# Kernel tuning notes

Measured on AMD Instinct MI355X. Metric: run time of the kernel, lower is better.

The kernel has to match this reference:

```python
import jax, jax.numpy as jnp
import numpy as np

D_MODEL = 1024
NUM_HEADS = 16
BATCH = 2
SEQ = 2048


def setup_inputs() -> dict:
    key = jax.random.key(0)
    ks = jax.random.split(key, 5)
    scale = 1.0 / np.sqrt(D_MODEL)
    x = jax.random.normal(ks[0], (BATCH, SEQ, D_MODEL), dtype=jnp.float32)
    Wq = jax.random.normal(ks[1], (D_MODEL, D_MODEL), dtype=jnp.float32) * scale
    Wk = jax.random.normal(ks[2], (D_MODEL, D_MODEL), dtype=jnp.float32) * scale
    Wv = jax.random.normal(ks[3], (D_MODEL, D_MODEL), dtype=jnp.float32) * scale
    Wo = jax.random.normal(ks[4], (D_MODEL, D_MODEL), dtype=jnp.float32) * scale
    return {"x": x, "Wq": Wq, "Wk": Wk, "Wv": Wv, "Wo": Wo}


def reference(x, Wq, Wk, Wv, Wo):
    b, s, d_model = x.shape
    h = NUM_HEADS
    d_head = d_model // h
    # projections (Linear with weight [out,in]: y = x @ W^T)
    def split_heads(y):
        return y.reshape(b, s, h, d_head).transpose(0, 2, 1, 3)  # b h s d
    q = split_heads(x @ Wq.T)
    k = split_heads(x @ Wk.T)
    v = split_heads(x @ Wv.T)
    # full (non-flash) attention, as in the original
    att = jnp.einsum('bhsd,bhtd->bhst', q, k) / jnp.sqrt(jnp.float32(d_head)).astype(x.dtype)
    att = jax.nn.softmax(att, axis=-1)
    out = jnp.einsum('bhst,bhtd->bhsd', att, v)
    out = out.transpose(0, 2, 1, 3).reshape(b, s, d_model)
    return out @ Wo.T
```

## Files before the change

kernel.cpp:

```cpp
#include <hip/hip_runtime.h>
#include <stdint.h>

typedef __bf16 bf16_t;
typedef __bf16 bf16x4 __attribute__((ext_vector_type(4)));
typedef __bf16 bf16x8 __attribute__((ext_vector_type(8)));
typedef float  f32x4  __attribute__((ext_vector_type(4)));
typedef float  f32x16 __attribute__((ext_vector_type(16)));

#define D_MODEL 1024
#define SEQ     2048
#define BATCH   2
#define NHEAD   16
#define DHEAD   64
#define NROWS   (BATCH*SEQ)
#define LDT     72

#define QSCALE  (0.125f * 1.4426950408889634f)

__device__ __forceinline__ void async_ld16(const bf16_t* g, bf16_t* l) {
    __builtin_amdgcn_global_load_lds(
        (const __attribute__((address_space(1))) uint32_t*)(uintptr_t)g,
        (__attribute__((address_space(3))) uint32_t*)(uintptr_t)l,
        16, 0, 0);
}

__device__ __forceinline__ bf16x8 cvt8(f32x4 lo, f32x4 hi) {
    bf16x8 o;
#pragma unroll
    for (int i = 0; i < 4; ++i) { o[i] = (bf16_t)lo[i]; o[4 + i] = (bf16_t)hi[i]; }
    return o;
}

__device__ __forceinline__ bf16x4 shflx32(bf16x4 v) {
    union { bf16x4 b; long long u; } x;
    x.b = v;
    x.u = __shfl_xor(x.u, 32);
    return x.b;
}

__global__ void __launch_bounds__(256)
k_cvt(const float* __restrict__ w0, const float* __restrict__ w1,
      const float* __restrict__ w2, const float* __restrict__ w3,
      const float* __restrict__ x,
      bf16_t* __restrict__ o0, bf16_t* __restrict__ o1,
      bf16_t* __restrict__ o2, bf16_t* __restrict__ o3,
      bf16_t* __restrict__ ox)
{
    const int blk = blockIdx.x;
    const float* s; bf16_t* d; int bi;
    if (blk < 2048) { s = x; d = ox; bi = blk; }
    else {
        const int t = blk - 2048, sel = t >> 9; bi = t & 511;
        s = (sel == 0) ? w0 : (sel == 1) ? w1 : (sel == 2) ? w2 : w3;
        d = (sel == 0) ? o0 : (sel == 1) ? o1 : (sel == 2) ? o2 : o3;
    }
    const size_t i = ((size_t)bi * 256 + threadIdx.x) * 8;
    *(bf16x8*)(d + i) = cvt8(*(const f32x4*)(s + i), *(const f32x4*)(s + i + 4));
}

template <int OUT_MODE>
__device__ __forceinline__ void gemm128(bf16_t* __restrict__ smem,
                                        const bf16_t* __restrict__ X,
                                        const bf16_t* __restrict__ W,
                                        void* __restrict__ Yv,
                                        int m0, int n0, float oscale)
{
    bf16_t* lA = smem;
    bf16_t* lB = smem + 128 * 32;

    const int tid  = threadIdx.x;
    const int lane = tid & 63;
    const int w    = tid >> 6;
    const int l15  = lane & 15;
    const int quad = lane >> 4;

    const int c0 = tid, c1 = tid + 256;
    const int r0 = c0 >> 2, r1 = c1 >> 2;
    const int kc0 = (c0 & 3) ^ ((r0 >> 1) & 3);
    const int kc1 = (c1 & 3) ^ ((r1 >> 1) & 3);
    const bf16_t* gA0 = X + (size_t)(m0 + r0) * D_MODEL + kc0 * 8;
    const bf16_t* gA1 = X + (size_t)(m0 + r1) * D_MODEL + kc1 * 8;
    const bf16_t* gB0 = W + (size_t)(n0 + r0) * D_MODEL + kc0 * 8;
    const bf16_t* gB1 = W + (size_t)(n0 + r1) * D_MODEL + kc1 * 8;

    int am[4], bn[4];
    const int mw = (w >> 1) * 64, nw = (w & 1) * 64;
#pragma unroll
    for (int i = 0; i < 4; ++i) {
        const int ra = mw + i * 16 + l15;
        am[i] = ra * 32 + (quad ^ ((ra >> 1) & 3)) * 8;
        const int rb = nw + i * 16 + l15;
        bn[i] = rb * 32 + (quad ^ ((rb >> 1) & 3)) * 8;
    }

    f32x4 acc[4][4];
#pragma unroll
    for (int i = 0; i < 4; ++i)
#pragma unroll
        for (int j = 0; j < 4; ++j) acc[i][j] = f32x4{0.f, 0.f, 0.f, 0.f};

    for (int k0 = 0; k0 < D_MODEL; k0 += 32) {
        __syncthreads();
        async_ld16(gA0 + k0, &lA[c0 * 8]);
        async_ld16(gA1 + k0, &lA[c1 * 8]);
        async_ld16(gB0 + k0, &lB[c0 * 8]);
        async_ld16(gB1 + k0, &lB[c1 * 8]);
        __syncthreads();

        bf16x8 af[4], bfr[4];
#pragma unroll
        for (int i = 0; i < 4; ++i) af[i]  = *(const bf16x8*)&lA[am[i]];
#pragma unroll
        for (int i = 0; i < 4; ++i) bfr[i] = *(const bf16x8*)&lB[bn[i]];
#pragma unroll
        for (int mi = 0; mi < 4; ++mi)
#pragma unroll
            for (int ni = 0; ni < 4; ++ni)
                acc[mi][ni] = __builtin_amdgcn_mfma_f32_16x16x32_bf16(
                    af[mi], bfr[ni], acc[mi][ni], 0, 0, 0);
    }

    if constexpr (OUT_MODE == 1) {
        bf16_t* lT = smem;
#pragma unroll
        for (int h0 = 0; h0 < 2; ++h0) {
            __syncthreads();
            if ((w >> 1) == h0) {
#pragma unroll
                for (int mi = 0; mi < 4; ++mi)
#pragma unroll
                    for (int ni = 0; ni < 4; ++ni) {
                        bf16x4 pk;
#pragma unroll
                        for (int r = 0; r < 4; ++r)
                            pk[r] = (bf16_t)(acc[mi][ni][r] * oscale);
                        const int col = nw + ni * 16 + l15;
                        *(bf16x4*)&lT[col * LDT + mi * 16 + quad * 4] = pk;
                    }
            }
            __syncthreads();
            const int col = tid & 127;
            const int seg = tid >> 7;
            const int brow = m0 + h0 * 64;
            const int b = brow >> 11, sb = brow & 2047;
            const int cg = n0 + col;
            bf16_t* dst = (bf16_t*)Yv +
                ((size_t)((b << 4) | (cg >> 6)) * 64 + (cg & 63)) * SEQ + sb;
#pragma unroll
            for (int u = 0; u < 4; ++u)
                *(bf16x8*)(dst + seg * 32 + u * 8) =
                    *(const bf16x8*)&lT[col * LDT + seg * 32 + u * 8];
        }
    } else {
#pragma unroll
        for (int mi = 0; mi < 4; ++mi)
#pragma unroll
            for (int ni = 0; ni < 4; ++ni)
#pragma unroll
                for (int r = 0; r < 4; ++r) {
                    const int row = m0 + mw + mi * 16 + quad * 4 + r;
                    const int col = n0 + nw + ni * 16 + l15;
                    const float vv = acc[mi][ni][r] * oscale;
                    if constexpr (OUT_MODE == 0)
                        ((bf16_t*)Yv)[(size_t)row * D_MODEL + col] = (bf16_t)vv;
                    else
                        ((float*)Yv)[(size_t)row * D_MODEL + col] = vv;
                }
    }
}

__global__ void __launch_bounds__(256, 3)
k_gemm_qkv(const bf16_t* __restrict__ X,
           const bf16_t* __restrict__ Wq, const bf16_t* __restrict__ Wk,
           const bf16_t* __restrict__ Wv,
           bf16_t* __restrict__ Qb, bf16_t* __restrict__ Kb, bf16_t* __restrict__ Vt)
{
    __shared__ __align__(16) bf16_t smem[128 * LDT];
    const int sel = blockIdx.y >> 3;
    const int n0  = (blockIdx.y & 7) * 128;
    const int m0  = blockIdx.x * 128;
    if (sel == 0)      gemm128<0>(smem, X, Wq, Qb, m0, n0, QSCALE);
    else if (sel == 1) gemm128<0>(smem, X, Wk, Kb, m0, n0, 1.0f);
    else               gemm128<1>(smem, X, Wv, Vt, m0, n0, 1.0f);
}

__global__ void __launch_bounds__(256, 3)
k_gemm_out(const bf16_t* __restrict__ X, const bf16_t* __restrict__ W,
           float* __restrict__ Y)
{
    __shared__ __align__(16) bf16_t smem[128 * LDT];
    gemm128<2>(smem, X, W, Y, blockIdx.x * 128, blockIdx.y * 128, 1.0f);
}

__global__ void __launch_bounds__(256, 2)
k_attn(const bf16_t* __restrict__ Qb, const bf16_t* __restrict__ Kb,
       const bf16_t* __restrict__ Vt, bf16_t* __restrict__ Ob)
{
    __shared__ __align__(16) bf16_t lK[2][64 * 64];
    __shared__ __align__(16) bf16_t lV[2][64 * 64];

    const int tid  = threadIdx.x;
    const int lane = tid & 63;
    const int w    = tid >> 6;
    const int l31  = lane & 31;
    const int h    = lane >> 5;

    const int bh = blockIdx.x;
    const int b_ = bh >> 4, hh = bh & 15;
    const int q0 = blockIdx.y * 128;

    const size_t base = (size_t)b_ * SEQ * D_MODEL + (size_t)hh * DHEAD;
    const bf16_t* Qp = Qb + base;
    const bf16_t* Kp = Kb + base;
    const bf16_t* Vp = Vt + (size_t)bh * DHEAD * SEQ;

    const int qrow = q0 + w * 32 + l31;
    bf16x8 qf[4];
#pragma unroll
    for (int c = 0; c < 4; ++c)
        qf[c] = *(const bf16x8*)&Qp[(size_t)qrow * D_MODEL + c * 16 + h * 8];

    const int c0 = tid, c1 = tid + 256;
    const int r0 = c0 >> 3, g0 = (c0 & 7) ^ (r0 & 7);
    const int r1 = r0 + 32;
    const bf16_t* gK0 = Kp + (size_t)r0 * D_MODEL + g0 * 8;
    const bf16_t* gK1 = Kp + (size_t)r1 * D_MODEL + g0 * 8;
    const bf16_t* gV0 = Vp + (size_t)r0 * SEQ + g0 * 8;
    const bf16_t* gV1 = Vp + (size_t)r1 * SEQ + g0 * 8;

    int koff[2][4];
#pragma unroll
    for (int half = 0; half < 2; ++half)
#pragma unroll
        for (int c = 0; c < 4; ++c) {
            const int row = half * 32 + l31;
            koff[half][c] = row * 64 + ((2 * c + h) ^ (row & 7)) * 8;
        }

    bf16x8 onef;
#pragma unroll
    for (int i = 0; i < 8; ++i) onef[i] = (bf16_t)1.0f;

    f32x16 acc_o[2];
    f32x16 acc_s;
#pragma unroll
    for (int i = 0; i < 16; ++i) { acc_o[0][i] = 0.f; acc_o[1][i] = 0.f; acc_s[i] = 0.f; }

    async_ld16(gK0, &lK[0][c0 * 8]);
    async_ld16(gK1, &lK[0][c1 * 8]);
    async_ld16(gV0, &lV[0][c0 * 8]);
    async_ld16(gV1, &lV[0][c1 * 8]);
    asm volatile("s_waitcnt vmcnt(0)\n\ts_barrier" ::: "memory");

    int cur = 0;
    const int NT = SEQ / 64;
    for (int t = 0; t < NT; ++t) {
        if (t + 1 < NT) {
            const int kv0 = (t + 1) * 64;
            async_ld16(gK0 + (size_t)kv0 * D_MODEL, &lK[cur ^ 1][c0 * 8]);
            async_ld16(gK1 + (size_t)kv0 * D_MODEL, &lK[cur ^ 1][c1 * 8]);
            async_ld16(gV0 + kv0, &lV[cur ^ 1][c0 * 8]);
            async_ld16(gV1 + kv0, &lV[cur ^ 1][c1 * 8]);
        }
        const bf16_t* lKc = lK[cur];
        const bf16_t* lVc = lV[cur];

        bf16x4 pk[2][4];
#pragma unroll
        for (int half = 0; half < 2; ++half) {
            f32x16 st;
#pragma unroll
            for (int i = 0; i < 16; ++i) st[i] = 0.f;
            __builtin_amdgcn_s_setprio(1);
#pragma unroll
            for (int c = 0; c < 4; ++c) {
                bf16x8 kf = *(const bf16x8*)&lKc[koff[half][c]];
                st = __builtin_amdgcn_mfma_f32_32x32x16_bf16(kf, qf[c], st, 0, 0, 0);
            }
            __builtin_amdgcn_s_setprio(0);
#pragma unroll
            for (int g = 0; g < 4; ++g)
#pragma unroll
                for (int r = 0; r < 4; ++r)
                    pk[half][g][r] = (bf16_t)__builtin_amdgcn_exp2f(st[g * 4 + r]);
        }

        bf16x4 pt[2][4];
#pragma unroll
        for (int half = 0; half < 2; ++half)
#pragma unroll
            for (int g = 0; g < 4; ++g) pt[half][g] = shflx32(pk[half][g]);

        bf16x8 pf[4];
#pragma unroll
        for (int c = 0; c < 4; ++c) {
            const int half = c >> 1, e = 2 * (c & 1);
            bf16x4 lo = h ? pt[half][e + 1] : pk[half][e];
            bf16x4 hi = h ? pk[half][e + 1] : pt[half][e];
#pragma unroll
            for (int i = 0; i < 4; ++i) { pf[c][i] = lo[i]; pf[c][4 + i] = hi[i]; }
        }

        __builtin_amdgcn_s_setprio(1);
#pragma unroll
        for (int c = 0; c < 4; ++c)
            acc_s = __builtin_amdgcn_mfma_f32_32x32x16_bf16(pf[c], onef, acc_s, 0, 0, 0);
#pragma unroll
        for (int a = 0; a < 2; ++a)
#pragma unroll
            for (int c = 0; c < 4; ++c) {
                bf16x8 vf = *(const bf16x8*)&lVc[koff[a][c]];
                acc_o[a] = __builtin_amdgcn_mfma_f32_32x32x16_bf16(
                    pf[c], vf, acc_o[a], 0, 0, 0);
            }
        __builtin_amdgcn_s_setprio(0);

        asm volatile("s_waitcnt vmcnt(0)\n\ts_barrier" ::: "memory");
        cur ^= 1;
    }

#pragma unroll
    for (int g = 0; g < 4; ++g)
#pragma unroll
        for (int r = 0; r < 4; ++r) {
            const float inv = 1.0f / acc_s[g * 4 + r];
            const int ql  = w * 32 + r + 8 * g + 4 * h;
            const size_t rb = (size_t)(b_ * SEQ + q0 + ql) * D_MODEL
                            + hh * DHEAD + l31;
            Ob[rb]      = (bf16_t)(acc_o[0][g * 4 + r] * inv);
            Ob[rb + 32] = (bf16_t)(acc_o[1][g * 4 + r] * inv);
        }
}

extern "C" void kernel_launch(void* const* d_in, const int* in_sizes, int n_in,
                              void* d_out, int out_size, void* d_ws, size_t ws_size,
                              hipStream_t stream)
{
    const float* x  = (const float*)d_in[0];
    const float* Wq = (const float*)d_in[1];
    const float* Wk = (const float*)d_in[2];
    const float* Wv = (const float*)d_in[3];
    const float* Wo = (const float*)d_in[4];
    float* out = (float*)d_out;

    const size_t wmat = (size_t)D_MODEL * D_MODEL;
    const size_t mat  = (size_t)NROWS * D_MODEL;
    bf16_t* Wqb = (bf16_t*)d_ws;
    bf16_t* Wkb = Wqb + wmat;
    bf16_t* Wvb = Wkb + wmat;
    bf16_t* Wob = Wvb + wmat;
    bf16_t* Xb  = Wob + wmat;
    bf16_t* Qb  = Xb + mat;
    bf16_t* Kb  = Qb + mat;
    bf16_t* Vt  = Kb + mat;
    bf16_t* Ab  = Qb;

    dim3 blk(256);
    k_cvt<<<dim3(4096), blk, 0, stream>>>(Wq, Wk, Wv, Wo, x, Wqb, Wkb, Wvb, Wob, Xb);
    k_gemm_qkv<<<dim3(32, 24), blk, 0, stream>>>(Xb, Wqb, Wkb, Wvb, Qb, Kb, Vt);
    k_attn<<<dim3(32, 16), blk, 0, stream>>>(Qb, Kb, Vt, Ab);
    k_gemm_out<<<dim3(32, 8), blk, 0, stream>>>(Ab, Wob, out);
}
```

Baseline: 181.9 us.

## Split attention waves into 2x2 query/key grid, swap shuffles for permlane32

Reorganizes the attention block's four waves into a 2x2 grid. Each wave now handles 64 query rows against half of each 64-key tile, so every K and V fragment read from LDS feeds two MFMAs. Partial output and row-sum accumulators from the two key-halves are combined through a shared-memory reduction before the final normalize and store. The cross-half P transpose now uses v_permlane32_swap instead of __shfl_xor with selects, which removes LDS-based shuffle traffic. The cost is more accumulator registers, a larger LDS arena and an extra reduction step with a barrier at the end.

```diff
diff --git a/kernel.cpp b/kernel.cpp
--- a/kernel.cpp
+++ b/kernel.cpp
@@ -31,11 +31,8 @@
     return o;
 }
 
-__device__ __forceinline__ bf16x4 shflx32(bf16x4 v) {
-    union { bf16x4 b; long long u; } x;
-    x.b = v;
-    x.u = __shfl_xor(x.u, 32);
-    return x.b;
+__device__ __forceinline__ void plswap(uint32_t& a, uint32_t& b) {
+    asm("v_permlane32_swap_b32 %0, %1" : "+v"(a), "+v"(b));
 }
 
 __global__ void __launch_bounds__(256)
@@ -196,12 +193,15 @@
 k_attn(const bf16_t* __restrict__ Qb, const bf16_t* __restrict__ Kb,
        const bf16_t* __restrict__ Vt, bf16_t* __restrict__ Ob)
 {
-    __shared__ __align__(16) bf16_t lK[2][64 * 64];
-    __shared__ __align__(16) bf16_t lV[2][64 * 64];
+    __shared__ __align__(16) char arena[51200];
+    bf16_t* lK = (bf16_t*)arena;
+    bf16_t* lV = (bf16_t*)(arena + 16384);
 
     const int tid  = threadIdx.x;
     const int lane = tid & 63;
     const int w    = tid >> 6;
+    const int wq   = w >> 1;
+    const int wk   = w & 1;
     const int l31  = lane & 31;
     const int h    = lane >> 5;
 
@@ -214,11 +214,14 @@
     const bf16_t* Kp = Kb + base;
     const bf16_t* Vp = Vt + (size_t)bh * DHEAD * SEQ;
 
-    const int qrow = q0 + w * 32 + l31;
-    bf16x8 qf[4];
-#pragma unroll
-    for (int c = 0; c < 4; ++c)
-        qf[c] = *(const bf16x8*)&Qp[(size_t)qrow * D_MODEL + c * 16 + h * 8];
+    bf16x8 qf[2][4];
+#pragma unroll
+    for (int qh = 0; qh < 2; ++qh) {
+        const int qrow = q0 + wq * 64 + qh * 32 + l31;
+#pragma unroll
+        for (int c = 0; c < 4; ++c)
+            qf[qh][c] = *(const bf16x8*)&Qp[(size_t)qrow * D_MODEL + c * 16 + h * 8];
+    }
 
     const int c0 = tid, c1 = tid + 256;
     const int r0 = c0 >> 3, g0 = (c0 & 7) ^ (r0 & 7);
@@ -228,28 +231,39 @@
     const bf16_t* gV0 = Vp + (size_t)r0 * SEQ + g0 * 8;
     const bf16_t* gV1 = Vp + (size_t)r1 * SEQ + g0 * 8;
 
-    int koff[2][4];
-#pragma unroll
-    for (int half = 0; half < 2; ++half)
-#pragma unroll
-        for (int c = 0; c < 4; ++c) {
-            const int row = half * 32 + l31;
-            koff[half][c] = row * 64 + ((2 * c + h) ^ (row & 7)) * 8;
+    int koff[4], voff[2][2];
+#pragma unroll
+    for (int c = 0; c < 4; ++c) {
+        const int row = wk * 32 + l31;
+        koff[c] = row * 64 + (((2 * c + h) ^ (row & 7)) * 8);
+    }
+#pragma unroll
+    for (int a = 0; a < 2; ++a)
+#pragma unroll
+        for (int ck = 0; ck < 2; ++ck) {
+            const int row = a * 32 + l31;
+            const int ch  = 4 * wk + 2 * ck + h;
+            voff[a][ck] = row * 64 + ((ch ^ (row & 7)) * 8);
         }
 
     bf16x8 onef;
 #pragma unroll
     for (int i = 0; i < 8; ++i) onef[i] = (bf16_t)1.0f;
 
-    f32x16 acc_o[2];
-    f32x16 acc_s;
-#pragma unroll
-    for (int i = 0; i < 16; ++i) { acc_o[0][i] = 0.f; acc_o[1][i] = 0.f; acc_s[i] = 0.f; }
-
-    async_ld16(gK0, &lK[0][c0 * 8]);
-    async_ld16(gK1, &lK[0][c1 * 8]);
-    async_ld16(gV0, &lV[0][c0 * 8]);
-    async_ld16(gV1, &lV[0][c1 * 8]);
+    f32x16 acc_o[2][2];
+    f32x16 acc_s[2];
+#pragma unroll
+    for (int qh = 0; qh < 2; ++qh) {
+#pragma unroll
+        for (int i = 0; i < 16; ++i) {
+            acc_o[qh][0][i] = 0.f; acc_o[qh][1][i] = 0.f; acc_s[qh][i] = 0.f;
+        }
+    }
+
+    async_ld16(gK0, &lK[c0 * 8]);
+    async_ld16(gK1, &lK[c1 * 8]);
+    async_ld16(gV0, &lV[c0 * 8]);
+    async_ld16(gV1, &lV[c1 * 8]);
     asm volatile("s_waitcnt vmcnt(0)\n\ts_barrier" ::: "memory");
 
     int cur = 0;
@@ -257,79 +271,133 @@
     for (int t = 0; t < NT; ++t) {
         if (t + 1 < NT) {
             const int kv0 = (t + 1) * 64;
-            async_ld16(gK0 + (size_t)kv0 * D_MODEL, &lK[cur ^ 1][c0 * 8]);
-            async_ld16(gK1 + (size_t)kv0 * D_MODEL, &lK[cur ^ 1][c1 * 8]);
-            async_ld16(gV0 + kv0, &lV[cur ^ 1][c0 * 8]);
-            async_ld16(gV1 + kv0, &lV[cur ^ 1][c1 * 8]);
-        }
-        const bf16_t* lKc = lK[cur];
-        const bf16_t* lVc = lV[cur];
+            const int nb = (cur ^ 1) * 4096;
+            async_ld16(gK0 + (size_t)kv0 * D_MODEL, &lK[nb + c0 * 8]);
+            async_ld16(gK1 + (size_t)kv0 * D_MODEL, &lK[nb + c1 * 8]);
+            async_ld16(gV0 + kv0, &lV[nb + c0 * 8]);
+            async_ld16(gV1 + kv0, &lV[nb + c1 * 8]);
+        }
+        const bf16_t* lKc = lK + cur * 4096;
+        const bf16_t* lVc = lV + cur * 4096;
+
+        bf16x8 kf[4];
+#pragma unroll
+        for (int c = 0; c < 4; ++c) kf[c] = *(const bf16x8*)&lKc[koff[c]];
+
+        f32x16 st[2];
+#pragma unroll
+        for (int qh = 0; qh < 2; ++qh)
+#pragma unroll
+            for (int i = 0; i < 16; ++i) st[qh][i] = 0.f;
+        __builtin_amdgcn_s_setprio(1);
+#pragma unroll
+        for (int qh = 0; qh < 2; ++qh)
+#pragma unroll
+            for (int c = 0; c < 4; ++c)
+                st[qh] = __builtin_amdgcn_mfma_f32_32x32x16_bf16(
+                    kf[c], qf[qh][c], st[qh], 0, 0, 0);
+        __builtin_amdgcn_s_setprio(0);
 
         bf16x4 pk[2][4];
 #pragma unroll
-        for (int half = 0; half < 2; ++half) {
-            f32x16 st;
-#pragma unroll
-            for (int i = 0; i < 16; ++i) st[i] = 0.f;
-            __builtin_amdgcn_s_setprio(1);
-#pragma unroll
-            for (int c = 0; c < 4; ++c) {
-                bf16x8 kf = *(const bf16x8*)&lKc[koff[half][c]];
-                st = __builtin_amdgcn_mfma_f32_32x32x16_bf16(kf, qf[c], st, 0, 0, 0);
+        for (int qh = 0; qh < 2; ++qh)
+#pragma unroll
+            for (int g = 0; g < 4; ++g)
+#pragma unroll
+                for (int r = 0; r < 4; ++r)
+                    pk[qh][g][r] = (bf16_t)__builtin_amdgcn_exp2f(st[qh][g * 4 + r]);
+
+        bf16x8 pf[2][2];
+#pragma unroll
+        for (int qh = 0; qh < 2; ++qh)
+#pragma unroll
+            for (int ck = 0; ck < 2; ++ck) {
+                union { bf16x4 v; uint32_t d[2]; } ua, ub;
+                ua.v = pk[qh][2 * ck];
+                ub.v = pk[qh][2 * ck + 1];
+                uint32_t a0 = ua.d[0], b0 = ub.d[0];
+                uint32_t a1 = ua.d[1], b1 = ub.d[1];
+                plswap(a0, b0);
+                plswap(a1, b1);
+                union { bf16x8 v; uint32_t d[4]; } up;
+                up.d[0] = a0; up.d[1] = a1; up.d[2] = b0; up.d[3] = b1;
+                pf[qh][ck] = up.v;
             }
-            __builtin_amdgcn_s_setprio(0);
-#pragma unroll
-            for (int g = 0; g < 4; ++g)
-#pragma unroll
-                for (int r = 0; r < 4; ++r)
-                    pk[half][g][r] = (bf16_t)__builtin_amdgcn_exp2f(st[g * 4 + r]);
-        }
-
-        bf16x4 pt[2][4];
-#pragma unroll
-        for (int half = 0; half < 2; ++half)
-#pragma unroll
-            for (int g = 0; g < 4; ++g) pt[half][g] = shflx32(pk[half][g]);
-
-        bf16x8 pf[4];
-#pragma unroll
-        for (int c = 0; c < 4; ++c) {
-            const int half = c >> 1, e = 2 * (c & 1);
-            bf16x4 lo = h ? pt[half][e + 1] : pk[half][e];
-            bf16x4 hi = h ? pk[half][e + 1] : pt[half][e];
-#pragma unroll
-            for (int i = 0; i < 4; ++i) { pf[c][i] = lo[i]; pf[c][4 + i] = hi[i]; }
-        }
 
         __builtin_amdgcn_s_setprio(1);
 #pragma unroll
-        for (int c = 0; c < 4; ++c)
-            acc_s = __builtin_amdgcn_mfma_f32_32x32x16_bf16(pf[c], onef, acc_s, 0, 0, 0);
+        for (int qh = 0; qh < 2; ++qh)
+#pragma unroll
+            for (int ck = 0; ck < 2; ++ck)
+                acc_s[qh] = __builtin_amdgcn_mfma_f32_32x32x16_bf16(
+                    pf[qh][ck], onef, acc_s[qh], 0, 0, 0);
 #pragma unroll
         for (int a = 0; a < 2; ++a)
 #pragma unroll
-            for (int c = 0; c < 4; ++c) {
-                bf16x8 vf = *(const bf16x8*)&lVc[koff[a][c]];
-                acc_o[a] = __builtin_amdgcn_mfma_f32_32x32x16_bf16(
-                    pf[c], vf, acc_o[a], 0, 0, 0);
+            for (int ck = 0; ck < 2; ++ck) {
+                bf16x8 vf = *(const bf16x8*)&lVc[voff[a][ck]];
+#pragma unroll
+                for (int qh = 0; qh < 2; ++qh)
+                    acc_o[qh][a] = __builtin_amdgcn_mfma_f32_32x32x16_bf16(
+                        pf[qh][ck], vf, acc_o[qh][a], 0, 0, 0);
             }
         __builtin_amdgcn_s_setprio(0);
 
-        asm volatile("s_waitcnt vmcnt(0)\n\ts_barrier" ::: "memory");
+        asm volatile("s_waitcnt vmcnt(0) lgkmcnt(0)\n\ts_barrier" ::: "memory");
         cur ^= 1;
     }
 
-#pragma unroll
-    for (int g = 0; g < 4; ++g)
-#pragma unroll
-        for (int r = 0; r < 4; ++r) {
-            const float inv = 1.0f / acc_s[g * 4 + r];
-            const int ql  = w * 32 + r + 8 * g + 4 * h;
-            const size_t rb = (size_t)(b_ * SEQ + q0 + ql) * D_MODEL
-                            + hh * DHEAD + l31;
-            Ob[rb]      = (bf16_t)(acc_o[0][g * 4 + r] * inv);
-            Ob[rb + 32] = (bf16_t)(acc_o[1][g * 4 + r] * inv);
-        }
+    union F16 { f32x16 v; f32x4 q[4]; };
+    float* blob = (float*)arena + ((size_t)(wq * 64 + lane)) * 100;
+
+    if (wk) {
+#pragma unroll
+        for (int qh = 0; qh < 2; ++qh) {
+#pragma unroll
+            for (int a = 0; a < 2; ++a) {
+                F16 u; u.v = acc_o[qh][a];
+#pragma unroll
+                for (int i = 0; i < 4; ++i)
+                    *(f32x4*)&blob[(qh * 8 + a * 4 + i) * 4] = u.q[i];
+            }
+            F16 s; s.v = acc_s[qh];
+#pragma unroll
+            for (int i = 0; i < 4; ++i)
+                *(f32x4*)&blob[64 + (qh * 4 + i) * 4] = s.q[i];
+        }
+    }
+    __syncthreads();
+    if (!wk) {
+#pragma unroll
+        for (int qh = 0; qh < 2; ++qh) {
+#pragma unroll
+            for (int a = 0; a < 2; ++a) {
+                F16 u; u.v = acc_o[qh][a];
+#pragma unroll
+                for (int i = 0; i < 4; ++i)
+                    u.q[i] += *(const f32x4*)&blob[(qh * 8 + a * 4 + i) * 4];
+                acc_o[qh][a] = u.v;
+            }
+            F16 s; s.v = acc_s[qh];
+#pragma unroll
+            for (int i = 0; i < 4; ++i)
+                s.q[i] += *(const f32x4*)&blob[64 + (qh * 4 + i) * 4];
+            acc_s[qh] = s.v;
+        }
+
+#pragma unroll
+        for (int qh = 0; qh < 2; ++qh)
+#pragma unroll
+            for (int g = 0; g < 4; ++g)
+#pragma unroll
+                for (int r = 0; r < 4; ++r) {
+                    const float inv = 1.0f / acc_s[qh][g * 4 + r];
+                    const int row = b_ * SEQ + q0 + wq * 64 + qh * 32 + (r + 8 * g + 4 * h);
+                    const size_t rb = (size_t)row * D_MODEL + hh * DHEAD + l31;
+                    Ob[rb]      = (bf16_t)(acc_o[qh][0][g * 4 + r] * inv);
+                    Ob[rb + 32] = (bf16_t)(acc_o[qh][1][g * 4 + r] * inv);
+                }
+    }
 }
 
 extern "C" void kernel_launch(void* const* d_in, const int* in_sizes, int n_in,
```

New measurement: 179.1 us. No clear change (-1.6%).
